# Kernel tuning notes

Measured on AMD Instinct MI355X. Metric: run time of the kernel, lower is better.

Reference implementation:

```python
import jax, jax.numpy as jnp
import numpy as np

TEMPERATURE = 0.5
EPS = 1e-12  # matches torch F.normalize eps


def _l2_normalize(x):
    norm = jnp.linalg.norm(x, axis=-1, keepdims=True)
    return x / jnp.maximum(norm, EPS)


def setup_inputs() -> dict:
    key = jax.random.key(0)
    k1, k2, k3 = jax.random.split(key, 3)
    N, D = 16384, 128
    self_predictions = jax.random.normal(k1, (N, D), dtype=jnp.float32)
    pos_predictions = jax.random.normal(k2, (N, D), dtype=jnp.float32)
    labels1 = jax.random.randint(k3, (N,), 0, 100, dtype=jnp.int64)
    return {
        "self_predictions": self_predictions,
        "pos_predictions": pos_predictions,
        "labels1": labels1,
    }


def reference(self_predictions, pos_predictions, labels1):
    N = labels1.shape[0]
    a = _l2_normalize(self_predictions)  # [N, D]
    b = _l2_normalize(pos_predictions)   # [N, D]
    # cosine similarity of already-normalized rows == dot product (GEMM form)
    sim = jnp.einsum("nd,md->nm", a, b)  # [N, N]
    neg_mask = (labels1[:, None] != labels1[None, :]).astype(sim.dtype)  # 1 - mask
    neg = jnp.exp(-sim / TEMPERATURE) * neg_mask
    return neg.sum() / (N * (N - 1))
```

## Files before the change

kernel.cpp:

```cpp
#include <hip/hip_runtime.h>

typedef unsigned char u8;
typedef unsigned short u16;
typedef float f32x4 __attribute__((ext_vector_type(4)));
typedef int i32x4 __attribute__((ext_vector_type(4)));
typedef int i32x8 __attribute__((ext_vector_type(8)));

#define NROWS 16384
#define DIM 128

#define NEG2LOG2E -2.8853900817779268f
#define SCALE ((float)(1.0 / (16384.0 * 16383.0)))

#define SCALE1 0x7F7F7F7F

#define KMAX 320
#define NCORR 100
#define NGEMM 4096

__global__ __launch_bounds__(256) void norm_kernel(
    const float* __restrict__ a, const float* __restrict__ b,
    u8* __restrict__ aO, u8* __restrict__ bO)
{
    int tid  = threadIdx.x;
    int lane = tid & 63;
    int w    = tid >> 6;
    int half = lane >> 5;
    int l32  = lane & 31;
    long row = (long)blockIdx.x * 8 + w * 2 + half;

    const float4 va = ((const float4*)(a + row * DIM))[l32];
    float sa = va.x * va.x + va.y * va.y + va.z * va.z + va.w * va.w;
    #pragma unroll
    for (int off = 16; off; off >>= 1) sa += __shfl_xor(sa, off, 64);
    float inva = 1.0f / fmaxf(sqrtf(sa), 1e-12f);
    int pa = __builtin_amdgcn_cvt_pk_fp8_f32(va.x * inva, va.y * inva, 0, false);
    pa = __builtin_amdgcn_cvt_pk_fp8_f32(va.z * inva, va.w * inva, pa, true);
    ((int*)(aO + row * DIM))[l32] = pa;

    const float4 vb = ((const float4*)(b + row * DIM))[l32];
    float sb = vb.x * vb.x + vb.y * vb.y + vb.z * vb.z + vb.w * vb.w;
    #pragma unroll
    for (int off = 16; off; off >>= 1) sb += __shfl_xor(sb, off, 64);
    float invb = NEG2LOG2E / fmaxf(sqrtf(sb), 1e-12f);
    int pb = __builtin_amdgcn_cvt_pk_fp8_f32(vb.x * invb, vb.y * invb, 0, false);
    pb = __builtin_amdgcn_cvt_pk_fp8_f32(vb.z * invb, vb.w * invb, pb, true);
    ((int*)(bO + row * DIM))[l32] = pb;
}

__global__ __launch_bounds__(256, 4) void gemm_kernel(
    const u8* __restrict__ A, const u8* __restrict__ B,
    const int* __restrict__ labels,
    float* __restrict__ partials, float* __restrict__ corrP)
{
    __shared__ u8 sB[2][16384];
    __shared__ float redS[4];
    __shared__ int sCnt;

    int tid  = threadIdx.x;
    int lane = tid & 63;
    int w    = tid >> 6;
    int mrow = lane & 15;
    int q    = lane >> 4;

    if (blockIdx.x < NCORR) {
        int l = blockIdx.x;
        int* sIdx = (int*)sB;
        if (tid == 0) sCnt = 0;
        __syncthreads();

        for (int i = tid; i < NROWS; i += 256)
            if (labels[i] == l) {
                int p = atomicAdd(&sCnt, 1);
                if (p < KMAX) sIdx[p] = i;
            }
        __syncthreads();

        int k = sCnt < KMAX ? sCnt : KMAX;
        int nt = (k + 15) >> 4;
        int ntk = nt << 4;
        for (int r = k + tid; r < ntk; r += 256) sIdx[r] = sIdx[0];
        __syncthreads();

        int npairs = nt * nt;
        float s = 0.0f;
        for (int tp = w; tp < npairs; tp += 8) {
            int tpB = tp + 4;
            bool has2 = tpB < npairs;
            int tp2 = has2 ? tpB : tp;

            int ti1 = tp / nt,  tj1 = tp  - ti1 * nt;
            int ti2 = tp2 / nt, tj2 = tp2 - ti2 * nt;
            int ri1 = sIdx[ti1 * 16 + mrow], rj1 = sIdx[tj1 * 16 + mrow];
            int ri2 = sIdx[ti2 * 16 + mrow], rj2 = sIdx[tj2 * 16 + mrow];

            const u8* pa1 = A + (size_t)ri1 * DIM + q * 32;
            const u8* pb1 = B + (size_t)rj1 * DIM + q * 32;
            const u8* pa2 = A + (size_t)ri2 * DIM + q * 32;
            const u8* pb2 = B + (size_t)rj2 * DIM + q * 32;

            i32x8 aF1, bF1, aF2, bF2;
            *((i32x4*)&aF1)     = *(const i32x4*)pa1;
            *((i32x4*)&aF1 + 1) = *(const i32x4*)(pa1 + 16);
            *((i32x4*)&bF1)     = *(const i32x4*)pb1;
            *((i32x4*)&bF1 + 1) = *(const i32x4*)(pb1 + 16);
            *((i32x4*)&aF2)     = *(const i32x4*)pa2;
            *((i32x4*)&aF2 + 1) = *(const i32x4*)(pa2 + 16);
            *((i32x4*)&bF2)     = *(const i32x4*)pb2;
            *((i32x4*)&bF2 + 1) = *(const i32x4*)(pb2 + 16);

            f32x4 acc1 = (f32x4){0.f, 0.f, 0.f, 0.f};
            f32x4 acc2 = (f32x4){0.f, 0.f, 0.f, 0.f};
            acc1 = __builtin_amdgcn_mfma_scale_f32_16x16x128_f8f6f4(
                aF1, bF1, acc1, 0, 0, 0, SCALE1, 0, SCALE1);
            acc2 = __builtin_amdgcn_mfma_scale_f32_16x16x128_f8f6f4(
                aF2, bF2, acc2, 0, 0, 0, SCALE1, 0, SCALE1);

            int i1 = ti1 * 16 + q * 4, j1 = tj1 * 16 + mrow;
            int i2 = ti2 * 16 + q * 4, j2 = tj2 * 16 + mrow;
            #pragma unroll
            for (int r = 0; r < 4; r++) {
                float e1 = __builtin_amdgcn_exp2f(acc1[r]);
                s += ((i1 + r) < k && j1 < k) ? e1 : 0.0f;
                float e2 = __builtin_amdgcn_exp2f(acc2[r]);
                s += (has2 && (i2 + r) < k && j2 < k) ? e2 : 0.0f;
            }
        }

        #pragma unroll
        for (int off = 32; off; off >>= 1) s += __shfl_xor(s, off, 64);
        if (lane == 0) redS[w] = s;
        __syncthreads();
        if (tid == 0)
            corrP[l] = (redS[0] + redS[1] + redS[2] + redS[3]) * SCALE;
        return;
    }

    int g  = blockIdx.x - NCORR;
    int wr = w >> 1;
    int wc = w & 1;

    int rowBase = (g >> 5) * 128;
    int colBase = (g & 31) * 512;

    int m0 = tid >> 3;
    int p0 = tid & 7;
    int srcOff = m0 * 128 + ((p0 ^ (m0 & 7)) << 4);
    int ldsOff = (tid - lane) * 16;

    const u8* gB = B + (size_t)colBase * DIM + srcOff;

    i32x8 a8[4];
    #pragma unroll
    for (int mi = 0; mi < 4; mi++) {
        const u8* pa = A + (size_t)(rowBase + wr * 64 + mi * 16 + mrow) * DIM
                         + q * 32;
        *((i32x4*)&a8[mi])     = *(const i32x4*)pa;
        *((i32x4*)&a8[mi] + 1) = *(const i32x4*)(pa + 16);
    }

    {
        const u8* gp = gB;
        u8* lp = &sB[0][ldsOff];
        #pragma unroll
        for (int it = 0; it < 4; it++) {
            __builtin_amdgcn_global_load_lds(
                (const __attribute__((address_space(1))) void*)gp,
                (__attribute__((address_space(3))) void*)lp, 16, 0, 0);
            gp += 4096; lp += 4096;
        }
    }

    int bOff[4];
    #pragma unroll
    for (int ni = 0; ni < 4; ni++) {
        int n = wc * 64 + ni * 16 + mrow;
        bOff[ni] = n * 128 + (((q << 1) ^ (n & 7)) << 4);
    }

    __syncthreads();

    const f32x4 z4 = (f32x4){0.f, 0.f, 0.f, 0.f};
    float s0 = 0.0f, s1 = 0.0f, s2 = 0.0f, s3 = 0.0f;

    #pragma unroll
    for (int jt = 0; jt < 4; jt++) {
        if (jt < 3) {
            const u8* gp = gB + (jt + 1) * (128 * DIM);
            u8* lp = &sB[(jt + 1) & 1][ldsOff];
            #pragma unroll
            for (int it = 0; it < 4; it++) {
                __builtin_amdgcn_global_load_lds(
                    (const __attribute__((address_space(1))) void*)gp,
                    (__attribute__((address_space(3))) void*)lp, 16, 0, 0);
                gp += 4096; lp += 4096;
            }
        }

        const u8* sb = sB[jt & 1];
        i32x8 b8[4];
        #pragma unroll
        for (int ni = 0; ni < 4; ni++) {
            *((i32x4*)&b8[ni])     = *(const i32x4*)(sb + bOff[ni]);
            *((i32x4*)&b8[ni] + 1) = *(const i32x4*)(sb + (bOff[ni] ^ 16));
        }

        f32x4 acc[4][4];
        #pragma unroll
        for (int mi = 0; mi < 4; mi++)
            #pragma unroll
            for (int ni = 0; ni < 4; ni++)
                acc[mi][ni] = __builtin_amdgcn_mfma_scale_f32_16x16x128_f8f6f4(
                    a8[mi], b8[ni], z4, 0, 0, 0, SCALE1, 0, SCALE1);

        #pragma unroll
        for (int mi = 0; mi < 4; mi++)
            #pragma unroll
            for (int ni = 0; ni < 4; ni++) {
                s0 += __builtin_amdgcn_exp2f(acc[mi][ni][0]);
                s1 += __builtin_amdgcn_exp2f(acc[mi][ni][1]);
                s2 += __builtin_amdgcn_exp2f(acc[mi][ni][2]);
                s3 += __builtin_amdgcn_exp2f(acc[mi][ni][3]);
            }

        if (jt < 3) __syncthreads();
    }

    float s = (s0 + s1) + (s2 + s3);
    #pragma unroll
    for (int off = 32; off; off >>= 1) s += __shfl_xor(s, off, 64);

    if (lane == 0) redS[w] = s;
    __syncthreads();
    if (tid == 0) {
        float t = (redS[0] + redS[1]) + (redS[2] + redS[3]);
        partials[g] = t * SCALE;
    }
}

__global__ __launch_bounds__(256) void reduce_kernel(
    const float* __restrict__ gP, const float* __restrict__ cP,
    float* __restrict__ out)
{
    int tid = threadIdx.x;
    const float4* p4 = (const float4*)gP;
    float s = 0.0f;
    #pragma unroll 4
    for (int i = tid; i < 1024; i += 256) {
        float4 v = p4[i];
        s += (v.x + v.y) + (v.z + v.w);
    }
    if (tid < NCORR) s -= cP[tid];
    #pragma unroll
    for (int off = 32; off; off >>= 1) s += __shfl_xor(s, off, 64);
    __shared__ float red[4];
    if ((tid & 63) == 0) red[tid >> 6] = s;
    __syncthreads();
    if (tid == 0) out[0] = (red[0] + red[1]) + (red[2] + red[3]);
}

extern "C" void kernel_launch(void* const* d_in, const int* in_sizes, int n_in,
                              void* d_out, int out_size, void* d_ws, size_t ws_size,
                              hipStream_t stream) {
    const float* self_p = (const float*)d_in[0];
    const float* pos_p  = (const float*)d_in[1];
    const int*   labels = (const int*)d_in[2];
    float* out = (float*)d_out;

    u8* aB = (u8*)d_ws;
    u8* bB = aB + (size_t)NROWS * DIM;
    float* gemmP = (float*)(bB + (size_t)NROWS * DIM);
    float* corrP = gemmP + NGEMM;

    norm_kernel<<<NROWS / 8, 256, 0, stream>>>(self_p, pos_p, aB, bB);
    gemm_kernel<<<NCORR + NGEMM, 256, 0, stream>>>(aB, bB, labels, gemmP, corrP);
    reduce_kernel<<<1, 256, 0, stream>>>(gemmP, corrP, out);
}
```

Baseline: 117.4 us.

## Load B fragments directly from global memory per wave, dropping LDS staging

The GEMM blocks no longer stage B tiles in double-buffered shared memory with barriers. Each wave now owns a 64x256 output tile and reads its B fragments straight from global memory (relying on L2/cache). This removes the LDS traffic and block-wide syncs, and the occupancy hint drops from 4 to 3. In exchange, B is no longer reused across waves through LDS, which raises global and cache load volume, and there is no explicit prefetch to hide load latency.

```diff
diff --git a/kernel.cpp b/kernel.cpp
--- a/kernel.cpp
+++ b/kernel.cpp
@@ -48,12 +48,12 @@
     ((int*)(bO + row * DIM))[l32] = pb;
 }
 
-__global__ __launch_bounds__(256, 4) void gemm_kernel(
+__global__ __launch_bounds__(256, 3) void gemm_kernel(
     const u8* __restrict__ A, const u8* __restrict__ B,
     const int* __restrict__ labels,
     float* __restrict__ partials, float* __restrict__ corrP)
 {
-    __shared__ u8 sB[2][16384];
+    __shared__ int sIdx[KMAX];
     __shared__ float redS[4];
     __shared__ int sCnt;
 
@@ -65,7 +65,6 @@
 
     if (blockIdx.x < NCORR) {
         int l = blockIdx.x;
-        int* sIdx = (int*)sB;
         if (tid == 0) sCnt = 0;
         __syncthreads();
 
@@ -137,72 +136,30 @@
     }
 
     int g  = blockIdx.x - NCORR;
-    int wr = w >> 1;
-    int wc = w & 1;
-
-    int rowBase = (g >> 5) * 128;
-    int colBase = (g & 31) * 512;
-
-    int m0 = tid >> 3;
-    int p0 = tid & 7;
-    int srcOff = m0 * 128 + ((p0 ^ (m0 & 7)) << 4);
-    int ldsOff = (tid - lane) * 16;
-
-    const u8* gB = B + (size_t)colBase * DIM + srcOff;
+    int gw = g * 4 + w;
+    int r0 = (gw & 255) * 64;
+    int c0 = (gw >> 8) * 256;
 
     i32x8 a8[4];
     #pragma unroll
     for (int mi = 0; mi < 4; mi++) {
-        const u8* pa = A + (size_t)(rowBase + wr * 64 + mi * 16 + mrow) * DIM
-                         + q * 32;
+        const u8* pa = A + (size_t)(r0 + mi * 16 + mrow) * DIM + q * 32;
         *((i32x4*)&a8[mi])     = *(const i32x4*)pa;
         *((i32x4*)&a8[mi] + 1) = *(const i32x4*)(pa + 16);
     }
 
-    {
-        const u8* gp = gB;
-        u8* lp = &sB[0][ldsOff];
-        #pragma unroll
-        for (int it = 0; it < 4; it++) {
-            __builtin_amdgcn_global_load_lds(
-                (const __attribute__((address_space(1))) void*)gp,
-                (__attribute__((address_space(3))) void*)lp, 16, 0, 0);
-            gp += 4096; lp += 4096;
-        }
-    }
-
-    int bOff[4];
-    #pragma unroll
-    for (int ni = 0; ni < 4; ni++) {
-        int n = wc * 64 + ni * 16 + mrow;
-        bOff[ni] = n * 128 + (((q << 1) ^ (n & 7)) << 4);
-    }
-
-    __syncthreads();
-
     const f32x4 z4 = (f32x4){0.f, 0.f, 0.f, 0.f};
     float s0 = 0.0f, s1 = 0.0f, s2 = 0.0f, s3 = 0.0f;
 
     #pragma unroll
-    for (int jt = 0; jt < 4; jt++) {
-        if (jt < 3) {
-            const u8* gp = gB + (jt + 1) * (128 * DIM);
-            u8* lp = &sB[(jt + 1) & 1][ldsOff];
-            #pragma unroll
-            for (int it = 0; it < 4; it++) {
-                __builtin_amdgcn_global_load_lds(
-                    (const __attribute__((address_space(1))) void*)gp,
-                    (__attribute__((address_space(3))) void*)lp, 16, 0, 0);
-                gp += 4096; lp += 4096;
-            }
-        }
-
-        const u8* sb = sB[jt & 1];
+    for (int ct = 0; ct < 4; ct++) {
+        const u8* pbBase = B + (size_t)(c0 + ct * 64 + mrow) * DIM + q * 32;
         i32x8 b8[4];
         #pragma unroll
         for (int ni = 0; ni < 4; ni++) {
-            *((i32x4*)&b8[ni])     = *(const i32x4*)(sb + bOff[ni]);
-            *((i32x4*)&b8[ni] + 1) = *(const i32x4*)(sb + (bOff[ni] ^ 16));
+            const u8* pb = pbBase + (size_t)(ni * 16) * DIM;
+            *((i32x4*)&b8[ni])     = *(const i32x4*)pb;
+            *((i32x4*)&b8[ni] + 1) = *(const i32x4*)(pb + 16);
         }
 
         f32x4 acc[4][4];
@@ -222,8 +179,6 @@
                 s2 += __builtin_amdgcn_exp2f(acc[mi][ni][2]);
                 s3 += __builtin_amdgcn_exp2f(acc[mi][ni][3]);
             }
-
-        if (jt < 3) __syncthreads();
     }
 
     float s = (s0 + s1) + (s2 + s3);
```

After: 155.7 us. 1.33x slower.
